# Kernel optimization log

Hardware: AMD Instinct MI355X
Metric: run time of the kernel (lower is better)

## Reference

```python
import jax, jax.numpy as jnp
import numpy as np

K = 3          # kernel_size
BOARD = 15     # gomoku board H = W
HOUT = BOARD - K + 1   # 13 windows per spatial dim
DIM_IN = 2 * K * K     # 18 binary features per window -> perfect hash


def fake_quant(x, scale, bits=8):
    """Straight-through fake quantization: round to int grid, clamp to bit range."""
    qmax = 2 ** (bits - 1) - 1
    y = jnp.clip(jnp.round(x * scale), -qmax - 1, qmax) / scale
    return x + jax.lax.stop_gradient(y - x)


def setup_inputs() -> dict:
    key = jax.random.key(0)
    ks = jax.random.split(key, 8)
    B = 8192
    board = jax.random.randint(ks[0], (B, 2, BOARD, BOARD), 0, 2, dtype=jnp.int32)
    emb = jax.random.normal(ks[1], (2 ** 18, 32), dtype=jnp.float32) * 0.05
    w1 = jax.random.normal(ks[2], (32, 32), dtype=jnp.float32) * 0.1
    b1 = jax.random.normal(ks[3], (32,), dtype=jnp.float32) * 0.05
    w2 = jax.random.normal(ks[4], (32, 32), dtype=jnp.float32) * 0.1
    b2 = jax.random.normal(ks[5], (32,), dtype=jnp.float32) * 0.05
    w3 = jax.random.normal(ks[6], (3, 32), dtype=jnp.float32) * 0.1
    b3 = jax.random.normal(ks[7], (3,), dtype=jnp.float32) * 0.05
    return {"board": board, "emb": emb, "w1": w1, "b1": b1,
            "w2": w2, "b2": b2, "w3": w3, "b3": b3}


def reference(board, emb, w1, b1, w2, b2, w3, b3):
    B = board.shape[0]
    # im2col unfold in torch F.unfold order (channel-major, then kernel row, col)
    # patches: (B, HOUT, HOUT, C*K*K)
    patches = jnp.stack(
        [board[:, c, i:i + HOUT, j:j + HOUT]
         for c in range(2) for i in range(K) for j in range(K)], axis=-1)
    # perfect hash of 18 binary features -> index into 2^18 embedding table
    powers = (2 ** jnp.arange(DIM_IN)).astype(jnp.int32)
    idx = jnp.sum(patches * powers, axis=-1)          # (B, HOUT, HOUT)
    feats = emb[idx]                                  # (B, HOUT, HOUT, 32) gather
    feats = fake_quant(jnp.clip(feats, -1.0, 127 / 128), 128.0, bits=8)
    v = jnp.sum(feats, axis=(1, 2))                   # (B, 32) clamp-sum accumulate
    # tiny quantized 3-layer value MLP
    for i, (wt, bs) in enumerate(((w1, b1), (w2, b2), (w3, b3))):
        v = jnp.clip(v, -1.0 if i == 0 else 0.0, 127 / 128)
        wq = fake_quant(wt, 128.0, bits=8)
        bq = fake_quant(bs, 128.0 * 128.0, bits=32)
        v = v @ wq.T + bq
    policy = jnp.zeros((B, BOARD, BOARD), dtype=v.dtype)
    return (v, policy)
```

## Files before the change

### kernel.cpp

```cpp
#include <hip/hip_runtime.h>
#include <stdint.h>

#define NW 169

typedef float f32x4 __attribute__((ext_vector_type(4)));

__device__ __forceinline__ float qw128(float x) {
    float r = rintf(x * 128.f);
    r = fminf(fmaxf(r, -128.f), 127.f);
    return r * 0.0078125f;
}
__device__ __forceinline__ float qb16384(float x) {
    return rintf(x * 16384.f) * 6.103515625e-05f;
}

__device__ __forceinline__ void quant_task(const float* __restrict__ emb,
                                           uint8_t* __restrict__ q, int task) {
    const float4* in4 = (const float4*)emb + (size_t)task * 4;
    uint32_t words[4];
#pragma unroll
    for (int t = 0; t < 4; ++t) {
        float4 f = in4[t];
        float v[4] = {f.x, f.y, f.z, f.w};
        uint32_t w = 0;
#pragma unroll
        for (int j = 0; j < 4; ++j) {
            float x = fminf(fmaxf(v[j], -1.f), 0.9921875f);
            int r = (int)rintf(x * 128.f) + 128;
            w |= ((uint32_t)r & 0xFFu) << (8 * j);
        }
        words[t] = w;
    }
    ((uint4*)q)[task] = make_uint4(words[0], words[1], words[2], words[3]);
}

__global__ void prep_kernel(const float* __restrict__ emb, uint8_t* __restrict__ q,
                            f32x4* __restrict__ policy) {
    int bid = blockIdx.x;
    int tid = threadIdx.x;
    if (bid >= 2048) {
        int i = (bid - 2048) * 256 + tid;
        f32x4 z = {0.f, 0.f, 0.f, 0.f};
        __builtin_nontemporal_store(z, &policy[i]);
        return;
    }
    quant_task(emb, q, bid * 256 + tid);
}

__global__ __launch_bounds__(256, 4)
void nnue_kernel(const int* __restrict__ board,
                 const uint8_t* __restrict__ embq,
                 const float* __restrict__ w1, const float* __restrict__ b1,
                 const float* __restrict__ w2, const float* __restrict__ b2,
                 const float* __restrict__ w3, const float* __restrict__ b3,
                 float* __restrict__ vout)
{
    __shared__ float w1T[32][32], w2T[32][32], w3T[32][4];
    __shared__ float b1q[32], b2q[32], b3q[4];
    __shared__ unsigned long long ballots[8][8];
    __shared__ int hashoff[8][192];
    __shared__ float vlds[8][32], h1lds[8][32], h2lds[8][32];

    int tid = threadIdx.x;
    for (int i = tid; i < 1024; i += 256) {
        int j = i & 31, k = i >> 5;
        w1T[k][j] = qw128(w1[j * 32 + k]);
        w2T[k][j] = qw128(w2[j * 32 + k]);
    }
    if (tid < 96) { int k = tid & 31, j = tid >> 5; w3T[k][j] = qw128(w3[j * 32 + k]); }
    if (tid < 32) { b1q[tid] = qb16384(b1[tid]); b2q[tid] = qb16384(b2[tid]); }
    if (tid < 3)  b3q[tid] = qb16384(b3[tid]);
    __syncthreads();

    int wv = tid >> 6, lane = tid & 63;
    int bbase = blockIdx.x * 8;
    int sA = wv * 2, sB = wv * 2 + 1;

#pragma unroll
    for (int rb = 0; rb < 2; ++rb) {
        int s = wv * 2 + rb;
        const int* bp = board + (size_t)(bbase + s) * 450;
#pragma unroll
        for (int t = 0; t < 8; ++t) {
            int n = t * 64 + lane;
            int cell = (n < 450) ? bp[n] : 0;
            unsigned long long m = __ballot(cell != 0);
            if (lane == 0) ballots[s][t] = m;
        }
#pragma unroll
        for (int t = 0; t < 3; ++t) {
            int w = t * 64 + lane;
            int wi = w / 13;
            int wj = w - wi * 13;
            int idx = 0;
#pragma unroll
            for (int c = 0; c < 2; ++c) {
#pragma unroll
                for (int i = 0; i < 3; ++i) {
                    int st = c * 225 + (min(wi, 12) + i) * 15;
                    int word = st >> 6, off = st & 63;
                    unsigned long long lo = ballots[s][word];
                    unsigned long long hi = ballots[s][word + 1];
                    unsigned long long bits = (lo >> off) | ((hi << 1) << (63 - off));
                    idx |= (int)((bits >> wj) & 7ull) << (9 * c + 3 * i);
                }
            }
            hashoff[s][w] = (w < NW) ? (idx << 5) : 0;
        }
    }

    int d1 = lane & 1;
    int g = lane >> 1;
    const uint8_t* base = embq + d1 * 16;
    uint4 dva[6], dvb[6];
#pragma unroll
    for (int it = 0; it < 6; ++it) dva[it] = *(const uint4*)(base + hashoff[sA][it * 32 + g]);
#pragma unroll
    for (int it = 0; it < 6; ++it) dvb[it] = *(const uint4*)(base + hashoff[sB][it * 32 + g]);

    const uint32_t M = 0x00FF00FFu;
    uint32_t keep5 = (160 + g < NW) ? 0xFFFFFFFFu : 0u;
    int jj = lane & 31, hf = lane >> 5;

    {
        uint32_t a0lo = 0, a0hi = 0, a1lo = 0, a1hi = 0;
        uint32_t a2lo = 0, a2hi = 0, a3lo = 0, a3hi = 0;
#pragma unroll
        for (int it = 0; it < 6; ++it) {
            uint32_t x0 = dva[it].x, x1 = dva[it].y, x2 = dva[it].z, x3 = dva[it].w;
            if (it == 5) { x0 &= keep5; x1 &= keep5; x2 &= keep5; x3 &= keep5; }
            a0lo += x0 & M; a0hi += (x0 >> 8) & M;
            a1lo += x1 & M; a1hi += (x1 >> 8) & M;
            a2lo += x2 & M; a2hi += (x2 >> 8) & M;
            a3lo += x3 & M; a3hi += (x3 >> 8) & M;
        }
#pragma unroll
        for (int off = 2; off <= 32; off <<= 1) {
            a0lo += __shfl_xor(a0lo, off); a0hi += __shfl_xor(a0hi, off);
            a1lo += __shfl_xor(a1lo, off); a1hi += __shfl_xor(a1hi, off);
            a2lo += __shfl_xor(a2lo, off); a2hi += __shfl_xor(a2hi, off);
            a3lo += __shfl_xor(a3lo, off); a3hi += __shfl_xor(a3hi, off);
        }
        if (lane < 2) {
            uint32_t lo[4] = {a0lo, a1lo, a2lo, a3lo};
            uint32_t hi[4] = {a0hi, a1hi, a2hi, a3hi};
#pragma unroll
            for (int j = 0; j < 4; ++j) {
                int c[4];
                c[0] = (int)(lo[j] & 0xFFFFu) - 21632;
                c[1] = (int)(hi[j] & 0xFFFFu) - 21632;
                c[2] = (int)(lo[j] >> 16)     - 21632;
                c[3] = (int)(hi[j] >> 16)     - 21632;
#pragma unroll
                for (int u = 0; u < 4; ++u) {
                    int cc = min(max(c[u], -128), 127);
                    vlds[sA][d1 * 16 + j * 4 + u] = (float)cc * 0.0078125f;
                }
            }
        }
        float t1 = 0.f;
#pragma unroll
        for (int k2 = 0; k2 < 16; ++k2) { int k = hf * 16 + k2; t1 = fmaf(vlds[sA][k], w1T[k][jj], t1); }
        t1 += __shfl_xor(t1, 32);
        t1 += b1q[jj];
        t1 = fminf(fmaxf(t1, 0.f), 0.9921875f);
        if (lane < 32) h1lds[sA][jj] = t1;

        float t2 = 0.f;
#pragma unroll
        for (int k2 = 0; k2 < 16; ++k2) { int k = hf * 16 + k2; t2 = fmaf(h1lds[sA][k], w2T[k][jj], t2); }
        t2 += __shfl_xor(t2, 32);
        t2 += b2q[jj];
        t2 = fminf(fmaxf(t2, 0.f), 0.9921875f);
        if (lane < 32) h2lds[sA][jj] = t2;

        float t3 = 0.f;
        if (jj < 3) {
#pragma unroll
            for (int k2 = 0; k2 < 16; ++k2) { int k = hf * 16 + k2; t3 = fmaf(h2lds[sA][k], w3T[k][jj], t3); }
        }
        t3 += __shfl_xor(t3, 32);
        if (lane < 3) vout[(size_t)(bbase + sA) * 3 + lane] = t3 + b3q[lane];
    }

    {
        uint32_t a0lo = 0, a0hi = 0, a1lo = 0, a1hi = 0;
        uint32_t a2lo = 0, a2hi = 0, a3lo = 0, a3hi = 0;
#pragma unroll
        for (int it = 0; it < 6; ++it) {
            uint32_t x0 = dvb[it].x, x1 = dvb[it].y, x2 = dvb[it].z, x3 = dvb[it].w;
            if (it == 5) { x0 &= keep5; x1 &= keep5; x2 &= keep5; x3 &= keep5; }
            a0lo += x0 & M; a0hi += (x0 >> 8) & M;
            a1lo += x1 & M; a1hi += (x1 >> 8) & M;
            a2lo += x2 & M; a2hi += (x2 >> 8) & M;
            a3lo += x3 & M; a3hi += (x3 >> 8) & M;
        }
#pragma unroll
        for (int off = 2; off <= 32; off <<= 1) {
            a0lo += __shfl_xor(a0lo, off); a0hi += __shfl_xor(a0hi, off);
            a1lo += __shfl_xor(a1lo, off); a1hi += __shfl_xor(a1hi, off);
            a2lo += __shfl_xor(a2lo, off); a2hi += __shfl_xor(a2hi, off);
            a3lo += __shfl_xor(a3lo, off); a3hi += __shfl_xor(a3hi, off);
        }
        if (lane < 2) {
            uint32_t lo[4] = {a0lo, a1lo, a2lo, a3lo};
            uint32_t hi[4] = {a0hi, a1hi, a2hi, a3hi};
#pragma unroll
            for (int j = 0; j < 4; ++j) {
                int c[4];
                c[0] = (int)(lo[j] & 0xFFFFu) - 21632;
                c[1] = (int)(hi[j] & 0xFFFFu) - 21632;
                c[2] = (int)(lo[j] >> 16)     - 21632;
                c[3] = (int)(hi[j] >> 16)     - 21632;
#pragma unroll
                for (int u = 0; u < 4; ++u) {
                    int cc = min(max(c[u], -128), 127);
                    vlds[sB][d1 * 16 + j * 4 + u] = (float)cc * 0.0078125f;
                }
            }
        }
        float t1 = 0.f;
#pragma unroll
        for (int k2 = 0; k2 < 16; ++k2) { int k = hf * 16 + k2; t1 = fmaf(vlds[sB][k], w1T[k][jj], t1); }
        t1 += __shfl_xor(t1, 32);
        t1 += b1q[jj];
        t1 = fminf(fmaxf(t1, 0.f), 0.9921875f);
        if (lane < 32) h1lds[sB][jj] = t1;

        float t2 = 0.f;
#pragma unroll
        for (int k2 = 0; k2 < 16; ++k2) { int k = hf * 16 + k2; t2 = fmaf(h1lds[sB][k], w2T[k][jj], t2); }
        t2 += __shfl_xor(t2, 32);
        t2 += b2q[jj];
        t2 = fminf(fmaxf(t2, 0.f), 0.9921875f);
        if (lane < 32) h2lds[sB][jj] = t2;

        float t3 = 0.f;
        if (jj < 3) {
#pragma unroll
            for (int k2 = 0; k2 < 16; ++k2) { int k = hf * 16 + k2; t3 = fmaf(h2lds[sB][k], w3T[k][jj], t3); }
        }
        t3 += __shfl_xor(t3, 32);
        if (lane < 3) vout[(size_t)(bbase + sB) * 3 + lane] = t3 + b3q[lane];
    }
}

extern "C" void kernel_launch(void* const* d_in, const int* in_sizes, int n_in,
                              void* d_out, int out_size, void* d_ws, size_t ws_size,
                              hipStream_t stream) {
    const int*   board = (const int*)d_in[0];
    const float* emb   = (const float*)d_in[1];
    const float* w1    = (const float*)d_in[2];
    const float* b1    = (const float*)d_in[3];
    const float* w2    = (const float*)d_in[4];
    const float* b2    = (const float*)d_in[5];
    const float* w3    = (const float*)d_in[6];
    const float* b3    = (const float*)d_in[7];
    float* out = (float*)d_out;
    uint8_t* embq = (uint8_t*)d_ws;

    prep_kernel<<<3848, 256, 0, stream>>>(emb, embq, (f32x4*)(out + 24576));
    nnue_kernel<<<1024, 256, 0, stream>>>(board, embq, w1, b1, w2, b2, w3, b3, out);
}
```

Baseline: 40.91 us.

## Move board bit-packing into prep kernel and bucket gathers by table half

The board ballot packing moves into the prep kernel as extra blocks, so it runs alongside the embedding quantization and writes 64-bit masks to workspace for the main kernel. Each board's window offsets are compacted into two lists by whether the offset falls in the low or high half of the quantized table. Gathers then go one half at a time in a loop, meant to improve cache locality of the random embedding reads. The cost is extra workspace traffic, ballot/popcount compaction work, and variable-trip loops replacing the fully unrolled, fully preloaded gather. The launch-bounds occupancy hint is also dropped.

Result: faster. 38.79 us (-5.2%).

```diff
diff --git a/kernel.cpp b/kernel.cpp
--- a/kernel.cpp
+++ b/kernel.cpp
@@ -14,41 +14,79 @@
     return rintf(x * 16384.f) * 6.103515625e-05f;
 }
 
-__device__ __forceinline__ void quant_task(const float* __restrict__ emb,
-                                           uint8_t* __restrict__ q, int task) {
-    const float4* in4 = (const float4*)emb + (size_t)task * 4;
-    uint32_t words[4];
-#pragma unroll
-    for (int t = 0; t < 4; ++t) {
-        float4 f = in4[t];
-        float v[4] = {f.x, f.y, f.z, f.w};
-        uint32_t w = 0;
-#pragma unroll
-        for (int j = 0; j < 4; ++j) {
-            float x = fminf(fmaxf(v[j], -1.f), 0.9921875f);
-            int r = (int)rintf(x * 128.f) + 128;
-            w |= ((uint32_t)r & 0xFFu) << (8 * j);
-        }
-        words[t] = w;
-    }
-    ((uint4*)q)[task] = make_uint4(words[0], words[1], words[2], words[3]);
-}
-
-__global__ void prep_kernel(const float* __restrict__ emb, uint8_t* __restrict__ q,
-                            f32x4* __restrict__ policy) {
-    int bid = blockIdx.x;
-    int tid = threadIdx.x;
+__global__ __launch_bounds__(256)
+void prep_kernel(const float* __restrict__ emb, uint8_t* __restrict__ q,
+                 f32x4* __restrict__ policy,
+                 const int* __restrict__ board, unsigned long long* __restrict__ bb)
+{
+    int bid = blockIdx.x, tid = threadIdx.x;
+    if (bid >= 3848) {
+        int wv = tid >> 6, lane = tid & 63;
+        int b = (bid - 3848) * 4 + wv;
+        const int* bp = board + (size_t)b * 450;
+#pragma unroll
+        for (int t = 0; t < 8; ++t) {
+            int n = t * 64 + lane;
+            int cell = (n < 450) ? bp[n] : 0;
+            unsigned long long m = __ballot(cell != 0);
+            if (lane == 0) bb[(size_t)b * 8 + t] = m;
+        }
+        return;
+    }
     if (bid >= 2048) {
         int i = (bid - 2048) * 256 + tid;
         f32x4 z = {0.f, 0.f, 0.f, 0.f};
         __builtin_nontemporal_store(z, &policy[i]);
         return;
     }
-    quant_task(emb, q, bid * 256 + tid);
-}
-
-__global__ __launch_bounds__(256, 4)
-void nnue_kernel(const int* __restrict__ board,
+    int i = bid * 256 + tid;
+    const float4* in4 = (const float4*)emb + (size_t)i * 4;
+    uint32_t words[4];
+#pragma unroll
+    for (int t = 0; t < 4; ++t) {
+        float4 f = in4[t];
+        float v[4] = {f.x, f.y, f.z, f.w};
+        uint32_t w = 0;
+#pragma unroll
+        for (int j = 0; j < 4; ++j) {
+            float x = fminf(fmaxf(v[j], -1.f), 0.9921875f);
+            int r = (int)rintf(x * 128.f) + 128;
+            w |= ((uint32_t)r & 0xFFu) << (8 * j);
+        }
+        words[t] = w;
+    }
+    ((uint4*)q)[i] = make_uint4(words[0], words[1], words[2], words[3]);
+}
+
+__device__ __forceinline__ void gather_pass(const int* lst, int cnt,
+        const uint8_t* __restrict__ tab, int lane,
+        uint32_t& a0lo, uint32_t& a0hi, uint32_t& a1lo, uint32_t& a1hi,
+        uint32_t& a2lo, uint32_t& a2hi, uint32_t& a3lo, uint32_t& a3hi)
+{
+    const uint32_t M = 0x00FF00FFu;
+    int half = lane >> 1;
+    for (int base = 0; base < cnt; base += 64) {
+        int i0 = base + half, i1 = i0 + 32;
+        int o0 = lst[min(i0, cnt - 1)];
+        int o1 = lst[min(i1, cnt - 1)];
+        uint4 e0 = *(const uint4*)(tab + o0);
+        uint4 e1 = *(const uint4*)(tab + o1);
+        uint32_t m0 = (i0 < cnt) ? 0xFFFFFFFFu : 0u;
+        uint32_t m1 = (i1 < cnt) ? 0xFFFFFFFFu : 0u;
+        uint32_t x;
+        x = e0.x & m0; a0lo += x & M; a0hi += (x >> 8) & M;
+        x = e1.x & m1; a0lo += x & M; a0hi += (x >> 8) & M;
+        x = e0.y & m0; a1lo += x & M; a1hi += (x >> 8) & M;
+        x = e1.y & m1; a1lo += x & M; a1hi += (x >> 8) & M;
+        x = e0.z & m0; a2lo += x & M; a2hi += (x >> 8) & M;
+        x = e1.z & m1; a2lo += x & M; a2hi += (x >> 8) & M;
+        x = e0.w & m0; a3lo += x & M; a3hi += (x >> 8) & M;
+        x = e1.w & m1; a3lo += x & M; a3hi += (x >> 8) & M;
+    }
+}
+
+__global__ __launch_bounds__(256)
+void nnue_kernel(const unsigned long long* __restrict__ bb,
                  const uint8_t* __restrict__ embq,
                  const float* __restrict__ w1, const float* __restrict__ b1,
                  const float* __restrict__ w2, const float* __restrict__ b2,
@@ -58,7 +96,7 @@
     __shared__ float w1T[32][32], w2T[32][32], w3T[32][4];
     __shared__ float b1q[32], b2q[32], b3q[4];
     __shared__ unsigned long long ballots[8][8];
-    __shared__ int hashoff[8][192];
+    __shared__ int list0[8][176], list1[8][176];
     __shared__ float vlds[8][32], h1lds[8][32], h2lds[8][32];
 
     int tid = threadIdx.x;
@@ -74,72 +112,62 @@
 
     int wv = tid >> 6, lane = tid & 63;
     int bbase = blockIdx.x * 8;
-    int sA = wv * 2, sB = wv * 2 + 1;
+    int sA = wv * 2, sB = sA + 1;
+    int c0A = 0, c1A = 0, c0B = 0, c1B = 0;
 
 #pragma unroll
     for (int rb = 0; rb < 2; ++rb) {
-        int s = wv * 2 + rb;
-        const int* bp = board + (size_t)(bbase + s) * 450;
-#pragma unroll
-        for (int t = 0; t < 8; ++t) {
-            int n = t * 64 + lane;
-            int cell = (n < 450) ? bp[n] : 0;
-            unsigned long long m = __ballot(cell != 0);
-            if (lane == 0) ballots[s][t] = m;
-        }
-#pragma unroll
-        for (int t = 0; t < 3; ++t) {
-            int w = t * 64 + lane;
-            int wi = w / 13;
-            int wj = w - wi * 13;
+        int s = sA + rb;
+        int b = bbase + s;
+        if (lane < 8) ballots[s][lane] = bb[(size_t)b * 8 + lane];
+        int cnt0 = 0, cnt1 = 0;
+#pragma unroll
+        for (int r = 0; r < 3; ++r) {
+            int w = r * 64 + lane;
+            bool valid = (w < NW);
+            int wc = min(w, NW - 1);
+            int wi = wc / 13, wj = wc - wi * 13;
             int idx = 0;
 #pragma unroll
             for (int c = 0; c < 2; ++c) {
 #pragma unroll
                 for (int i = 0; i < 3; ++i) {
-                    int st = c * 225 + (min(wi, 12) + i) * 15;
-                    int word = st >> 6, off = st & 63;
+                    int st = c * 225 + (wi + i) * 15;
+                    int word = st >> 6, o = st & 63;
                     unsigned long long lo = ballots[s][word];
                     unsigned long long hi = ballots[s][word + 1];
-                    unsigned long long bits = (lo >> off) | ((hi << 1) << (63 - off));
+                    unsigned long long bits = (lo >> o) | ((hi << 1) << (63 - o));
                     idx |= (int)((bits >> wj) & 7ull) << (9 * c + 3 * i);
                 }
             }
-            hashoff[s][w] = (w < NW) ? (idx << 5) : 0;
-        }
+            int off = idx << 5;
+            bool low = off < (1 << 22);
+            unsigned long long mlow = __ballot(valid && low);
+            unsigned long long mhig = __ballot(valid && !low);
+            unsigned long long lt = (1ull << lane) - 1ull;
+            if (valid && low)  list0[s][cnt0 + (int)__popcll(mlow & lt)] = off;
+            if (valid && !low) list1[s][cnt1 + (int)__popcll(mhig & lt)] = off;
+            cnt0 += (int)__popcll(mlow);
+            cnt1 += (int)__popcll(mhig);
+        }
+        if (rb == 0) { c0A = cnt0; c1A = cnt1; } else { c0B = cnt0; c1B = cnt1; }
     }
 
     int d1 = lane & 1;
-    int g = lane >> 1;
-    const uint8_t* base = embq + d1 * 16;
-    uint4 dva[6], dvb[6];
-#pragma unroll
-    for (int it = 0; it < 6; ++it) dva[it] = *(const uint4*)(base + hashoff[sA][it * 32 + g]);
-#pragma unroll
-    for (int it = 0; it < 6; ++it) dvb[it] = *(const uint4*)(base + hashoff[sB][it * 32 + g]);
-
-    const uint32_t M = 0x00FF00FFu;
-    uint32_t keep5 = (160 + g < NW) ? 0xFFFFFFFFu : 0u;
+    const uint8_t* tab = embq + d1 * 16;
     int jj = lane & 31, hf = lane >> 5;
 
     {
         uint32_t a0lo = 0, a0hi = 0, a1lo = 0, a1hi = 0;
         uint32_t a2lo = 0, a2hi = 0, a3lo = 0, a3hi = 0;
-#pragma unroll
-        for (int it = 0; it < 6; ++it) {
-            uint32_t x0 = dva[it].x, x1 = dva[it].y, x2 = dva[it].z, x3 = dva[it].w;
-            if (it == 5) { x0 &= keep5; x1 &= keep5; x2 &= keep5; x3 &= keep5; }
-            a0lo += x0 & M; a0hi += (x0 >> 8) & M;
-            a1lo += x1 & M; a1hi += (x1 >> 8) & M;
-            a2lo += x2 & M; a2hi += (x2 >> 8) & M;
-            a3lo += x3 & M; a3hi += (x3 >> 8) & M;
-        }
-#pragma unroll
-        for (int off = 2; off <= 32; off <<= 1) {
-            a0lo += __shfl_xor(a0lo, off); a0hi += __shfl_xor(a0hi, off);
-            a1lo += __shfl_xor(a1lo, off); a1hi += __shfl_xor(a1hi, off);
-            a2lo += __shfl_xor(a2lo, off); a2hi += __shfl_xor(a2hi, off);
-            a3lo += __shfl_xor(a3lo, off); a3hi += __shfl_xor(a3hi, off);
+        gather_pass(list0[sA], c0A, tab, lane, a0lo, a0hi, a1lo, a1hi, a2lo, a2hi, a3lo, a3hi);
+        gather_pass(list1[sA], c1A, tab, lane, a0lo, a0hi, a1lo, a1hi, a2lo, a2hi, a3lo, a3hi);
+#pragma unroll
+        for (int o = 2; o <= 32; o <<= 1) {
+            a0lo += __shfl_xor(a0lo, o); a0hi += __shfl_xor(a0hi, o);
+            a1lo += __shfl_xor(a1lo, o); a1hi += __shfl_xor(a1hi, o);
+            a2lo += __shfl_xor(a2lo, o); a2hi += __shfl_xor(a2hi, o);
+            a3lo += __shfl_xor(a3lo, o); a3hi += __shfl_xor(a3hi, o);
         }
         if (lane < 2) {
             uint32_t lo[4] = {a0lo, a1lo, a2lo, a3lo};
@@ -186,21 +214,14 @@
     {
         uint32_t a0lo = 0, a0hi = 0, a1lo = 0, a1hi = 0;
         uint32_t a2lo = 0, a2hi = 0, a3lo = 0, a3hi = 0;
-#pragma unroll
-        for (int it = 0; it < 6; ++it) {
-            uint32_t x0 = dvb[it].x, x1 = dvb[it].y, x2 = dvb[it].z, x3 = dvb[it].w;
-            if (it == 5) { x0 &= keep5; x1 &= keep5; x2 &= keep5; x3 &= keep5; }
-            a0lo += x0 & M; a0hi += (x0 >> 8) & M;
-            a1lo += x1 & M; a1hi += (x1 >> 8) & M;
-            a2lo += x2 & M; a2hi += (x2 >> 8) & M;
-            a3lo += x3 & M; a3hi += (x3 >> 8) & M;
-        }
-#pragma unroll
-        for (int off = 2; off <= 32; off <<= 1) {
-            a0lo += __shfl_xor(a0lo, off); a0hi += __shfl_xor(a0hi, off);
-            a1lo += __shfl_xor(a1lo, off); a1hi += __shfl_xor(a1hi, off);
-            a2lo += __shfl_xor(a2lo, off); a2hi += __shfl_xor(a2hi, off);
-            a3lo += __shfl_xor(a3lo, off); a3hi += __shfl_xor(a3hi, off);
+        gather_pass(list0[sB], c0B, tab, lane, a0lo, a0hi, a1lo, a1hi, a2lo, a2hi, a3lo, a3hi);
+        gather_pass(list1[sB], c1B, tab, lane, a0lo, a0hi, a1lo, a1hi, a2lo, a2hi, a3lo, a3hi);
+#pragma unroll
+        for (int o = 2; o <= 32; o <<= 1) {
+            a0lo += __shfl_xor(a0lo, o); a0hi += __shfl_xor(a0hi, o);
+            a1lo += __shfl_xor(a1lo, o); a1hi += __shfl_xor(a1hi, o);
+            a2lo += __shfl_xor(a2lo, o); a2hi += __shfl_xor(a2hi, o);
+            a3lo += __shfl_xor(a3lo, o); a3hi += __shfl_xor(a3hi, o);
         }
         if (lane < 2) {
             uint32_t lo[4] = {a0lo, a1lo, a2lo, a3lo};
@@ -258,7 +279,8 @@
     const float* b3    = (const float*)d_in[7];
     float* out = (float*)d_out;
     uint8_t* embq = (uint8_t*)d_ws;
-
-    prep_kernel<<<3848, 256, 0, stream>>>(emb, embq, (f32x4*)(out + 24576));
-    nnue_kernel<<<1024, 256, 0, stream>>>(board, embq, w1, b1, w2, b2, w3, b3, out);
-}
+    unsigned long long* bb = (unsigned long long*)(embq + (1u << 23));
+
+    prep_kernel<<<5896, 256, 0, stream>>>(emb, embq, (f32x4*)(out + 24576), board, bb);
+    nnue_kernel<<<1024, 256, 0, stream>>>(bb, embq, w1, b1, w2, b2, w3, b3, out);
+}
```
